# Optimization experiments

Measured on AMD Instinct MI355X. Metric: run time of the kernel, lower is better.

## Reference

```python
import jax, jax.numpy as jnp
import numpy as np

LOG_2PI = float(np.log(2.0 * np.pi))


def setup_inputs() -> dict:
    key = jax.random.key(0)
    k1, k2, k3 = jax.random.split(key, 3)
    N, M, D = 8192, 4096, 784
    samples = jax.random.normal(k1, (N, D), dtype=jnp.float32)
    x = jax.random.normal(k2, (M, D), dtype=jnp.float32)
    # per-feature std, kept away from zero for numerical sanity
    std = jax.random.uniform(k3, (D,), dtype=jnp.float32, minval=0.5, maxval=1.5)
    return {"samples": samples, "x": x, "std": std}


def reference(samples, x, std):
    # Diagonal-Gaussian mixture log-prob:
    #   logp[n, m] = sum_d [ -0.5*((s_nd - x_md)/std_d)^2 - 0.5*log(2*pi) - log(std_d) ]
    # computed via the ||u||^2 + ||v||^2 - 2 u.v identity on std-scaled vectors
    # (mathematically identical to the torch broadcast, without the (N,M,D) tensor).
    N, D = samples.shape
    M = x.shape[0]
    u = samples / std  # (N, D)
    v = x / std        # (M, D)
    sq_dist = (
        jnp.sum(u * u, axis=1)[:, None]
        + jnp.sum(v * v, axis=1)[None, :]
        - 2.0 * jnp.einsum("nd,md->nm", u, v)
    )  # (N, M)
    log_const = -0.5 * D * LOG_2PI - jnp.sum(jnp.log(std))
    log_prob = -0.5 * sq_dist + log_const  # (N, M)
    # logsumexp over mixture components, minus log(M)
    return jax.nn.logsumexp(log_prob, axis=1) - jnp.log(jnp.asarray(M, dtype=samples.dtype))
```

## Files before the change

kernel.cpp:

```cpp
#include <hip/hip_runtime.h>
#include <cstdint>
#include <cstddef>


#define N_ROWS 8192
#define M_ROWS 4096
#define D_DIM  784
#define KPB    896
#define LOG2PI 1.8378770664093453f
#define LOGM   8.317766166719343f

typedef unsigned char u8;
typedef __attribute__((ext_vector_type(8))) int   i32x8;
typedef __attribute__((ext_vector_type(4))) float f32x4;

__device__ __forceinline__ void gld16(const u8* g, u8* l) {
    __builtin_amdgcn_global_load_lds(
        (__attribute__((address_space(1))) void*)(void*)g,
        (__attribute__((address_space(3))) void*)l, 16, 0, 0);
}

__global__ __launch_bounds__(256) void k_prep(const float* __restrict__ samples,
                                              const float* __restrict__ x,
                                              const float* __restrict__ stdv,
                                              u8* __restrict__ dst,
                                              float* __restrict__ norm) {
    const int wid = threadIdx.x >> 6, lane = threadIdx.x & 63;
    const int row0 = blockIdx.x * 8 + wid * 2;

    float4 rstd[4];
#pragma unroll
    for (int i = 0; i < 4; ++i) {
        int c = lane + 64 * i;
        rstd[i] = make_float4(1.f, 1.f, 1.f, 1.f);
        if (c < 196) {
            float4 d = ((const float4*)stdv)[c];
            rstd[i] = make_float4(1.f / d.x, 1.f / d.y, 1.f / d.z, 1.f / d.w);
        }
    }

#pragma unroll
    for (int rr = 0; rr < 2; ++rr) {
        const int row = row0 + rr;
        const float* src = (row < N_ROWS) ? samples + (size_t)row * D_DIM
                                          : x + (size_t)(row - N_ROWS) * D_DIM;
        unsigned* drow = (unsigned*)(dst + (size_t)row * KPB);
        float sq = 0.f;
#pragma unroll
        for (int i = 0; i < 4; ++i) {
            const int c = lane + 64 * i;
            if (c < 224) {
                unsigned p = 0;
                if (c < 196) {
                    float4 s = ((const float4*)src)[c];
                    float ux = s.x * rstd[i].x, uy = s.y * rstd[i].y;
                    float uz = s.z * rstd[i].z, uw = s.w * rstd[i].w;
                    p = __builtin_amdgcn_cvt_pk_fp8_f32(ux, uy, 0, false);
                    p = __builtin_amdgcn_cvt_pk_fp8_f32(uz, uw, p, true);
                    float r0 = __builtin_amdgcn_cvt_f32_fp8(p, 0);
                    float r1 = __builtin_amdgcn_cvt_f32_fp8(p, 1);
                    float r2 = __builtin_amdgcn_cvt_f32_fp8(p, 2);
                    float r3 = __builtin_amdgcn_cvt_f32_fp8(p, 3);
                    sq += r0 * r0 + r1 * r1 + r2 * r2 + r3 * r3;
                }
                drow[c] = p;
            }
        }
        for (int m = 32; m; m >>= 1) sq += __shfl_xor(sq, m);
        if (lane == 0) norm[row] = sq;
    }
}

__global__ __launch_bounds__(256) void k_gemm(const u8* __restrict__ U,
                                              const u8* __restrict__ V,
                                              const float* __restrict__ vnorm,
                                              float* __restrict__ pmax,
                                              float* __restrict__ psum) {
    __shared__ __align__(16) char smem[65536];
    float2* part = (float2*)smem;

    const int tid = threadIdx.x;
    const int lane = tid & 63;
    const int wid = tid >> 6;
    const int waveRow = wid >> 1;
    const int waveCol = wid & 1;
    const int bCol = blockIdx.x;
    const int bRow = blockIdx.y;
    const int g = lane >> 4, rl = lane & 15;

    const int r16 = lane >> 2, sl = lane & 3;
    const int gc16 = sl ^ ((r16 >> 1) & 3);
    const u8* ga[4]; const u8* gb[4]; int loff[4];
#pragma unroll
    for (int t = 0; t < 4; ++t) {
        const int lin = wid * 4 + t, h = lin & 1, rg = lin >> 1;
        ga[t] = U + (size_t)(bRow * 128 + rg * 16 + r16) * KPB + h * 64 + gc16 * 16;
        gb[t] = V + (size_t)(bCol * 128 + rg * 16 + r16) * KPB + h * 64 + gc16 * 16;
        loff[t] = h * 8192 + rg * 1024;
    }

    const int key = (rl >> 1) & 3;
    const int hA = (g >> 1) * 8192;
    const int slotLo = (2 * (g & 1)) ^ key;
    const int aoff = hA + (waveRow * 64 + rl) * 64 + slotLo * 16;
    const int boff = 16384 + hA + (waveCol * 64 + rl) * 64 + slotLo * 16;

    f32x4 acc[4][4];
#pragma unroll
    for (int i = 0; i < 4; ++i)
#pragma unroll
        for (int j = 0; j < 4; ++j) acc[i][j] = (f32x4){0.f, 0.f, 0.f, 0.f};

#pragma unroll
    for (int t = 0; t < 4; ++t) gld16(ga[t], (u8*)(smem + loff[t]));
#pragma unroll
    for (int t = 0; t < 4; ++t) gld16(gb[t], (u8*)(smem + 16384 + loff[t]));

#pragma unroll
    for (int kt = 0; kt < 7; ++kt) {
        if (kt < 6) {
            char* nb = smem + ((kt + 1) & 1) * 32768;
            const int k1 = (kt + 1) * 128;
#pragma unroll
            for (int t = 0; t < 4; ++t) gld16(ga[t] + k1, (u8*)(nb + loff[t]));
#pragma unroll
            for (int t = 0; t < 4; ++t) gld16(gb[t] + k1, (u8*)(nb + 16384 + loff[t]));
            __builtin_amdgcn_s_waitcnt(0x0F78);
        } else {
            __builtin_amdgcn_s_waitcnt(0x0F70);
        }
        __builtin_amdgcn_s_barrier();

        const char* base = smem + (kt & 1) * 32768;
        i32x8 a[4], b[4];
#pragma unroll
        for (int i = 0; i < 4; ++i) {
            int4 L = *(const int4*)(base + (aoff + i * 1024));
            int4 H = *(const int4*)(base + ((aoff + i * 1024) ^ 16));
            a[i] = (i32x8){L.x, L.y, L.z, L.w, H.x, H.y, H.z, H.w};
        }
#pragma unroll
        for (int j = 0; j < 4; ++j) {
            int4 L = *(const int4*)(base + (boff + j * 1024));
            int4 H = *(const int4*)(base + ((boff + j * 1024) ^ 16));
            b[j] = (i32x8){L.x, L.y, L.z, L.w, H.x, H.y, H.z, H.w};
        }
#pragma unroll
        for (int i = 0; i < 4; ++i)
#pragma unroll
            for (int j = 0; j < 4; ++j)
                acc[i][j] = __builtin_amdgcn_mfma_scale_f32_16x16x128_f8f6f4(
                    a[i], b[j], acc[i][j], 0 , 0 ,
                    0, 127 , 0, 127 );

        __builtin_amdgcn_s_barrier();
    }
    __syncthreads();

    float vn[4];
#pragma unroll
    for (int j = 0; j < 4; ++j) vn[j] = vnorm[bCol * 128 + waveCol * 64 + j * 16 + rl];

    const int prow0 = waveRow * 64 + g * 4;
    const int pcol = waveCol * 16 + rl;
#pragma unroll
    for (int i = 0; i < 4; ++i) {
#pragma unroll
        for (int rg = 0; rg < 4; ++rg) {
            float w0 = acc[i][0][rg] - 0.5f * vn[0];
            float w1 = acc[i][1][rg] - 0.5f * vn[1];
            float w2 = acc[i][2][rg] - 0.5f * vn[2];
            float w3 = acc[i][3][rg] - 0.5f * vn[3];
            float m = fmaxf(fmaxf(w0, w1), fmaxf(w2, w3));
            float s = __expf(w0 - m) + __expf(w1 - m) + __expf(w2 - m) + __expf(w3 - m);
            part[(prow0 + i * 16 + rg) * 33 + pcol] = make_float2(m, s);
        }
    }
    __syncthreads();
    if (tid < 128) {
        const float2* p = part + tid * 33;
        float m = p[0].x;
#pragma unroll
        for (int c = 1; c < 32; ++c) m = fmaxf(m, p[c].x);
        float s = 0.f;
#pragma unroll
        for (int c = 0; c < 32; ++c) { float2 q = p[c]; s += q.y * __expf(q.x - m); }
        size_t grow = (size_t)(bRow * 128 + tid);
        pmax[grow * 32 + bCol] = m;
        psum[grow * 32 + bCol] = s;
    }
}

__global__ __launch_bounds__(256) void k_final(const float* __restrict__ pmax,
                                               const float* __restrict__ psum,
                                               const float* __restrict__ norm,
                                               const float* __restrict__ stdv,
                                               float* __restrict__ out) {
    __shared__ float wsum[4];
    const int t = threadIdx.x;
    float ls = 0.f;
    for (int d = t; d < D_DIM; d += 256) ls += logf(stdv[d]);
    for (int m = 32; m; m >>= 1) ls += __shfl_xor(ls, m);
    if ((t & 63) == 0) wsum[t >> 6] = ls;
    __syncthreads();
    const float logc = -0.5f * (float)D_DIM * LOG2PI - (wsum[0] + wsum[1] + wsum[2] + wsum[3]);

    const int n = blockIdx.x * 256 + t;
    const float* pm = pmax + (size_t)n * 32;
    const float* ps = psum + (size_t)n * 32;
    float gm = pm[0];
#pragma unroll
    for (int c = 1; c < 32; ++c) gm = fmaxf(gm, pm[c]);
    float S = 0.f;
#pragma unroll
    for (int c = 0; c < 32; ++c) S += ps[c] * __expf(pm[c] - gm);
    out[n] = gm + logf(S) - 0.5f * norm[n] + logc - LOGM;
}

extern "C" void kernel_launch(void* const* d_in, const int* in_sizes, int n_in,
                              void* d_out, int out_size, void* d_ws, size_t ws_size,
                              hipStream_t stream) {
    const float* samples = (const float*)d_in[0];
    const float* x       = (const float*)d_in[1];
    const float* stdv    = (const float*)d_in[2];
    float* out = (float*)d_out;

    char* ws = (char*)d_ws;
    u8*    U    = (u8*)ws;
    u8*    V    = (u8*)(ws + 7340032);
    float* norm = (float*)(ws + 11010048);
    float* pmax = (float*)(ws + 11059200);
    float* psum = (float*)(ws + 12107776);

    k_prep<<<(N_ROWS + M_ROWS) / 8, 256, 0, stream>>>(samples, x, stdv, U, norm);
    k_gemm<<<dim3(M_ROWS / 128, N_ROWS / 128), 256, 0, stream>>>(U, V, norm + N_ROWS, pmax, psum);
    k_final<<<N_ROWS / 256, 256, 0, stream>>>(pmax, psum, norm, stdv, out);
}
```

Before: 124.3 us.

## Enlarge GEMM tile to 256x256 with single-buffered LDS and shuffle-based epilogue

The fused FP8 GEMM+logsumexp kernel moves from 128x128 to 256x256 block tiles, with each wave computing a 128x128 sub-tile (8x8 MFMA accumulators). This raises arithmetic intensity and data reuse. LDS double buffering is replaced by a single buffer: fragments are loaded into registers, then the next K-slice is prefetched while the MFMAs run. The epilogue now reduces max and sum with cross-lane shuffles and writes per-wave partials directly instead of staging them in LDS. The grid becomes 16x32 = 512 blocks, at most one per CU under the launch bounds, and each thread holds 256 accumulator floats, so register spilling and low occupancy are real risks.

```diff
diff --git a/kernel.cpp b/kernel.cpp
--- a/kernel.cpp
+++ b/kernel.cpp
@@ -71,123 +71,110 @@
     }
 }
 
-__global__ __launch_bounds__(256) void k_gemm(const u8* __restrict__ U,
-                                              const u8* __restrict__ V,
-                                              const float* __restrict__ vnorm,
-                                              float* __restrict__ pmax,
-                                              float* __restrict__ psum) {
+__global__ __launch_bounds__(256, 1) void k_gemm(const u8* __restrict__ U,
+                                                 const u8* __restrict__ V,
+                                                 const float* __restrict__ vnorm,
+                                                 float* __restrict__ pmax,
+                                                 float* __restrict__ psum) {
     __shared__ __align__(16) char smem[65536];
-    float2* part = (float2*)smem;
 
     const int tid = threadIdx.x;
     const int lane = tid & 63;
     const int wid = tid >> 6;
-    const int waveRow = wid >> 1;
-    const int waveCol = wid & 1;
+    const int wRow = wid >> 1;
+    const int wCol = wid & 1;
     const int bCol = blockIdx.x;
     const int bRow = blockIdx.y;
     const int g = lane >> 4, rl = lane & 15;
 
-    const int r16 = lane >> 2, sl = lane & 3;
-    const int gc16 = sl ^ ((r16 >> 1) & 3);
-    const u8* ga[4]; const u8* gb[4]; int loff[4];
-#pragma unroll
-    for (int t = 0; t < 4; ++t) {
-        const int lin = wid * 4 + t, h = lin & 1, rg = lin >> 1;
-        ga[t] = U + (size_t)(bRow * 128 + rg * 16 + r16) * KPB + h * 64 + gc16 * 16;
-        gb[t] = V + (size_t)(bCol * 128 + rg * 16 + r16) * KPB + h * 64 + gc16 * 16;
-        loff[t] = h * 8192 + rg * 1024;
-    }
-
-    const int key = (rl >> 1) & 3;
-    const int hA = (g >> 1) * 8192;
-    const int slotLo = (2 * (g & 1)) ^ key;
-    const int aoff = hA + (waveRow * 64 + rl) * 64 + slotLo * 16;
-    const int boff = 16384 + hA + (waveCol * 64 + rl) * 64 + slotLo * 16;
-
-    f32x4 acc[4][4];
-#pragma unroll
-    for (int i = 0; i < 4; ++i)
-#pragma unroll
-        for (int j = 0; j < 4; ++j) acc[i][j] = (f32x4){0.f, 0.f, 0.f, 0.f};
-
-#pragma unroll
-    for (int t = 0; t < 4; ++t) gld16(ga[t], (u8*)(smem + loff[t]));
-#pragma unroll
-    for (int t = 0; t < 4; ++t) gld16(gb[t], (u8*)(smem + 16384 + loff[t]));
+    const int sr = lane >> 3;
+    const int gc16 = (lane & 7) ^ (2 * (sr & 3));
+    const u8* gaB = U + (size_t)(bRow * 256 + wid * 64 + sr) * KPB + gc16 * 16;
+    const u8* gbB = V + (size_t)(bCol * 256 + wid * 64 + sr) * KPB + gc16 * 16;
+    u8* laB = (u8*)(smem + wid * 8192);
+    u8* lbB = (u8*)(smem + 32768 + wid * 8192);
+
+    const int q = g ^ (rl & 3);
+    const int aoff = rl * 128 + q * 32;
+    const char* aB = smem + wRow * 16384;
+    const char* bB = smem + 32768 + wCol * 16384;
+
+    f32x4 acc[8][8];
+#pragma unroll
+    for (int i = 0; i < 8; ++i)
+#pragma unroll
+        for (int j = 0; j < 8; ++j) acc[i][j] = (f32x4){0.f, 0.f, 0.f, 0.f};
+
+#pragma unroll
+    for (int t = 0; t < 8; ++t) gld16(gaB + (size_t)t * 8 * KPB, laB + t * 1024);
+#pragma unroll
+    for (int t = 0; t < 8; ++t) gld16(gbB + (size_t)t * 8 * KPB, lbB + t * 1024);
 
 #pragma unroll
     for (int kt = 0; kt < 7; ++kt) {
+        __builtin_amdgcn_s_waitcnt(0x0F70);
+        __builtin_amdgcn_s_barrier();
+
+        i32x8 a[8], b[8];
+#pragma unroll
+        for (int i = 0; i < 8; ++i) {
+            int4 L = *(const int4*)(aB + aoff + i * 2048);
+            int4 H = *(const int4*)(aB + aoff + i * 2048 + 16);
+            a[i] = (i32x8){L.x, L.y, L.z, L.w, H.x, H.y, H.z, H.w};
+        }
+#pragma unroll
+        for (int j = 0; j < 8; ++j) {
+            int4 L = *(const int4*)(bB + aoff + j * 2048);
+            int4 H = *(const int4*)(bB + aoff + j * 2048 + 16);
+            b[j] = (i32x8){L.x, L.y, L.z, L.w, H.x, H.y, H.z, H.w};
+        }
+        __builtin_amdgcn_s_waitcnt(0xC07F);
+        __builtin_amdgcn_s_barrier();
+
         if (kt < 6) {
-            char* nb = smem + ((kt + 1) & 1) * 32768;
             const int k1 = (kt + 1) * 128;
 #pragma unroll
-            for (int t = 0; t < 4; ++t) gld16(ga[t] + k1, (u8*)(nb + loff[t]));
-#pragma unroll
-            for (int t = 0; t < 4; ++t) gld16(gb[t] + k1, (u8*)(nb + 16384 + loff[t]));
-            __builtin_amdgcn_s_waitcnt(0x0F78);
-        } else {
-            __builtin_amdgcn_s_waitcnt(0x0F70);
-        }
-        __builtin_amdgcn_s_barrier();
-
-        const char* base = smem + (kt & 1) * 32768;
-        i32x8 a[4], b[4];
-#pragma unroll
-        for (int i = 0; i < 4; ++i) {
-            int4 L = *(const int4*)(base + (aoff + i * 1024));
-            int4 H = *(const int4*)(base + ((aoff + i * 1024) ^ 16));
-            a[i] = (i32x8){L.x, L.y, L.z, L.w, H.x, H.y, H.z, H.w};
-        }
-#pragma unroll
-        for (int j = 0; j < 4; ++j) {
-            int4 L = *(const int4*)(base + (boff + j * 1024));
-            int4 H = *(const int4*)(base + ((boff + j * 1024) ^ 16));
-            b[j] = (i32x8){L.x, L.y, L.z, L.w, H.x, H.y, H.z, H.w};
-        }
-#pragma unroll
-        for (int i = 0; i < 4; ++i)
-#pragma unroll
-            for (int j = 0; j < 4; ++j)
+            for (int t = 0; t < 8; ++t) gld16(gaB + (size_t)t * 8 * KPB + k1, laB + t * 1024);
+#pragma unroll
+            for (int t = 0; t < 8; ++t) gld16(gbB + (size_t)t * 8 * KPB + k1, lbB + t * 1024);
+        }
+
+#pragma unroll
+        for (int i = 0; i < 8; ++i)
+#pragma unroll
+            for (int j = 0; j < 8; ++j)
                 acc[i][j] = __builtin_amdgcn_mfma_scale_f32_16x16x128_f8f6f4(
                     a[i], b[j], acc[i][j], 0 , 0 ,
                     0, 127 , 0, 127 );
-
-        __builtin_amdgcn_s_barrier();
-    }
-    __syncthreads();
-
-    float vn[4];
-#pragma unroll
-    for (int j = 0; j < 4; ++j) vn[j] = vnorm[bCol * 128 + waveCol * 64 + j * 16 + rl];
-
-    const int prow0 = waveRow * 64 + g * 4;
-    const int pcol = waveCol * 16 + rl;
-#pragma unroll
-    for (int i = 0; i < 4; ++i) {
-#pragma unroll
-        for (int rg = 0; rg < 4; ++rg) {
-            float w0 = acc[i][0][rg] - 0.5f * vn[0];
-            float w1 = acc[i][1][rg] - 0.5f * vn[1];
-            float w2 = acc[i][2][rg] - 0.5f * vn[2];
-            float w3 = acc[i][3][rg] - 0.5f * vn[3];
-            float m = fmaxf(fmaxf(w0, w1), fmaxf(w2, w3));
-            float s = __expf(w0 - m) + __expf(w1 - m) + __expf(w2 - m) + __expf(w3 - m);
-            part[(prow0 + i * 16 + rg) * 33 + pcol] = make_float2(m, s);
-        }
-    }
-    __syncthreads();
-    if (tid < 128) {
-        const float2* p = part + tid * 33;
-        float m = p[0].x;
-#pragma unroll
-        for (int c = 1; c < 32; ++c) m = fmaxf(m, p[c].x);
-        float s = 0.f;
-#pragma unroll
-        for (int c = 0; c < 32; ++c) { float2 q = p[c]; s += q.y * __expf(q.x - m); }
-        size_t grow = (size_t)(bRow * 128 + tid);
-        pmax[grow * 32 + bCol] = m;
-        psum[grow * 32 + bCol] = s;
+    }
+
+    float vn[8];
+#pragma unroll
+    for (int j = 0; j < 8; ++j) vn[j] = vnorm[bCol * 256 + wCol * 128 + j * 16 + rl];
+
+#pragma unroll
+    for (int i = 0; i < 8; ++i) {
+#pragma unroll
+        for (int r = 0; r < 4; ++r) {
+            float w[8];
+#pragma unroll
+            for (int j = 0; j < 8; ++j) w[j] = acc[i][j][r] - 0.5f * vn[j];
+            float m = w[0];
+#pragma unroll
+            for (int j = 1; j < 8; ++j) m = fmaxf(m, w[j]);
+#pragma unroll
+            for (int msk = 1; msk < 16; msk <<= 1) m = fmaxf(m, __shfl_xor(m, msk));
+            float s = 0.f;
+#pragma unroll
+            for (int j = 0; j < 8; ++j) s += __expf(w[j] - m);
+#pragma unroll
+            for (int msk = 1; msk < 16; msk <<= 1) s += __shfl_xor(s, msk);
+            if (rl == 0) {
+                size_t grow = (size_t)(bRow * 256 + wRow * 128 + i * 16 + g * 4 + r);
+                pmax[grow * 32 + bCol * 2 + wCol] = m;
+                psum[grow * 32 + bCol * 2 + wCol] = s;
+            }
+        }
     }
 }
 
@@ -233,6 +220,6 @@
     float* psum = (float*)(ws + 12107776);
 
     k_prep<<<(N_ROWS + M_ROWS) / 8, 256, 0, stream>>>(samples, x, stdv, U, norm);
-    k_gemm<<<dim3(M_ROWS / 128, N_ROWS / 128), 256, 0, stream>>>(U, V, norm + N_ROWS, pmax, psum);
+    k_gemm<<<dim3(M_ROWS / 256, N_ROWS / 256), 256, 0, stream>>>(U, V, norm + N_ROWS, pmax, psum);
     k_final<<<N_ROWS / 256, 256, 0, stream>>>(pmax, psum, norm, stdv, out);
 }
```

Result: slower. 273.5 us (+120.0%).

## Load A operand directly into registers, stage only B through LDS

Applied to the files above, without the earlier changes.

The GEMM kernel no longer stages the U (A) tile through shared memory. Each wave loads its A fragments straight from global memory into double-buffered registers, while only the V (B) tile goes through LDS. This halves LDS use, which could raise occupancy, and drops the A-side LDS reads, at the cost of uncoalesced 16-byte global loads and more registers. The prep kernel also changes to one row per wave, dividing by std directly instead of precomputing reciprocals, and launches twice as many blocks.

```diff
diff --git a/kernel.cpp b/kernel.cpp
--- a/kernel.cpp
+++ b/kernel.cpp
@@ -26,49 +26,34 @@
                                               u8* __restrict__ dst,
                                               float* __restrict__ norm) {
     const int wid = threadIdx.x >> 6, lane = threadIdx.x & 63;
-    const int row0 = blockIdx.x * 8 + wid * 2;
-
-    float4 rstd[4];
+    const int row = blockIdx.x * 4 + wid;
+    const float* src = (row < N_ROWS) ? samples + (size_t)row * D_DIM
+                                      : x + (size_t)(row - N_ROWS) * D_DIM;
+    unsigned* drow = (unsigned*)(dst + (size_t)row * KPB);
+    float sq = 0.f;
 #pragma unroll
     for (int i = 0; i < 4; ++i) {
-        int c = lane + 64 * i;
-        rstd[i] = make_float4(1.f, 1.f, 1.f, 1.f);
-        if (c < 196) {
-            float4 d = ((const float4*)stdv)[c];
-            rstd[i] = make_float4(1.f / d.x, 1.f / d.y, 1.f / d.z, 1.f / d.w);
-        }
-    }
-
-#pragma unroll
-    for (int rr = 0; rr < 2; ++rr) {
-        const int row = row0 + rr;
-        const float* src = (row < N_ROWS) ? samples + (size_t)row * D_DIM
-                                          : x + (size_t)(row - N_ROWS) * D_DIM;
-        unsigned* drow = (unsigned*)(dst + (size_t)row * KPB);
-        float sq = 0.f;
-#pragma unroll
-        for (int i = 0; i < 4; ++i) {
-            const int c = lane + 64 * i;
-            if (c < 224) {
-                unsigned p = 0;
-                if (c < 196) {
-                    float4 s = ((const float4*)src)[c];
-                    float ux = s.x * rstd[i].x, uy = s.y * rstd[i].y;
-                    float uz = s.z * rstd[i].z, uw = s.w * rstd[i].w;
-                    p = __builtin_amdgcn_cvt_pk_fp8_f32(ux, uy, 0, false);
-                    p = __builtin_amdgcn_cvt_pk_fp8_f32(uz, uw, p, true);
-                    float r0 = __builtin_amdgcn_cvt_f32_fp8(p, 0);
-                    float r1 = __builtin_amdgcn_cvt_f32_fp8(p, 1);
-                    float r2 = __builtin_amdgcn_cvt_f32_fp8(p, 2);
-                    float r3 = __builtin_amdgcn_cvt_f32_fp8(p, 3);
-                    sq += r0 * r0 + r1 * r1 + r2 * r2 + r3 * r3;
-                }
-                drow[c] = p;
+        const int c = lane + 64 * i;
+        if (c < 224) {
+            unsigned p = 0;
+            if (c < 196) {
+                float4 s = ((const float4*)src)[c];
+                float4 d = ((const float4*)stdv)[c];
+                float ux = s.x / d.x, uy = s.y / d.y;
+                float uz = s.z / d.z, uw = s.w / d.w;
+                p = __builtin_amdgcn_cvt_pk_fp8_f32(ux, uy, 0, false);
+                p = __builtin_amdgcn_cvt_pk_fp8_f32(uz, uw, p, true);
+                float r0 = __builtin_amdgcn_cvt_f32_fp8(p, 0);
+                float r1 = __builtin_amdgcn_cvt_f32_fp8(p, 1);
+                float r2 = __builtin_amdgcn_cvt_f32_fp8(p, 2);
+                float r3 = __builtin_amdgcn_cvt_f32_fp8(p, 3);
+                sq += r0 * r0 + r1 * r1 + r2 * r2 + r3 * r3;
             }
-        }
-        for (int m = 32; m; m >>= 1) sq += __shfl_xor(sq, m);
-        if (lane == 0) norm[row] = sq;
-    }
+            drow[c] = p;
+        }
+    }
+    for (int m = 32; m; m >>= 1) sq += __shfl_xor(sq, m);
+    if (lane == 0) norm[row] = sq;
 }
 
 __global__ __launch_bounds__(256) void k_gemm(const u8* __restrict__ U,
@@ -76,7 +61,7 @@
                                               const float* __restrict__ vnorm,
                                               float* __restrict__ pmax,
                                               float* __restrict__ psum) {
-    __shared__ __align__(16) char smem[65536];
+    __shared__ __align__(16) char smem[33792];
     float2* part = (float2*)smem;
 
     const int tid = threadIdx.x;
@@ -90,20 +75,20 @@
 
     const int r16 = lane >> 2, sl = lane & 3;
     const int gc16 = sl ^ ((r16 >> 1) & 3);
-    const u8* ga[4]; const u8* gb[4]; int loff[4];
+    const u8* gb[4]; int loffB[4];
 #pragma unroll
     for (int t = 0; t < 4; ++t) {
         const int lin = wid * 4 + t, h = lin & 1, rg = lin >> 1;
-        ga[t] = U + (size_t)(bRow * 128 + rg * 16 + r16) * KPB + h * 64 + gc16 * 16;
         gb[t] = V + (size_t)(bCol * 128 + rg * 16 + r16) * KPB + h * 64 + gc16 * 16;
-        loff[t] = h * 8192 + rg * 1024;
+        loffB[t] = h * 8192 + rg * 1024;
     }
 
     const int key = (rl >> 1) & 3;
-    const int hA = (g >> 1) * 8192;
+    const int hB = (g >> 1) * 8192;
     const int slotLo = (2 * (g & 1)) ^ key;
-    const int aoff = hA + (waveRow * 64 + rl) * 64 + slotLo * 16;
-    const int boff = 16384 + hA + (waveCol * 64 + rl) * 64 + slotLo * 16;
+    const int boff = hB + (waveCol * 64 + rl) * 64 + slotLo * 16;
+
+    const u8* gA = U + (size_t)(bRow * 128 + waveRow * 64 + rl) * KPB + g * 32;
 
     f32x4 acc[4][4];
 #pragma unroll
@@ -111,34 +96,34 @@
 #pragma unroll
         for (int j = 0; j < 4; ++j) acc[i][j] = (f32x4){0.f, 0.f, 0.f, 0.f};
 
-#pragma unroll
-    for (int t = 0; t < 4; ++t) gld16(ga[t], (u8*)(smem + loff[t]));
-#pragma unroll
-    for (int t = 0; t < 4; ++t) gld16(gb[t], (u8*)(smem + 16384 + loff[t]));
+    int4 aL[2][4], aH[2][4];
+
+#pragma unroll
+    for (int t = 0; t < 4; ++t) gld16(gb[t], (u8*)(smem + loffB[t]));
+#pragma unroll
+    for (int i = 0; i < 4; ++i) {
+        aL[0][i] = *(const int4*)(gA + (size_t)i * 16 * KPB);
+        aH[0][i] = *(const int4*)(gA + (size_t)i * 16 * KPB + 16);
+    }
 
 #pragma unroll
     for (int kt = 0; kt < 7; ++kt) {
+        const int cur = kt & 1, nxt = cur ^ 1;
+        __syncthreads();
         if (kt < 6) {
-            char* nb = smem + ((kt + 1) & 1) * 32768;
             const int k1 = (kt + 1) * 128;
 #pragma unroll
-            for (int t = 0; t < 4; ++t) gld16(ga[t] + k1, (u8*)(nb + loff[t]));
-#pragma unroll
-            for (int t = 0; t < 4; ++t) gld16(gb[t] + k1, (u8*)(nb + 16384 + loff[t]));
-            __builtin_amdgcn_s_waitcnt(0x0F78);
-        } else {
-            __builtin_amdgcn_s_waitcnt(0x0F70);
-        }
-        __builtin_amdgcn_s_barrier();
-
-        const char* base = smem + (kt & 1) * 32768;
-        i32x8 a[4], b[4];
-#pragma unroll
-        for (int i = 0; i < 4; ++i) {
-            int4 L = *(const int4*)(base + (aoff + i * 1024));
-            int4 H = *(const int4*)(base + ((aoff + i * 1024) ^ 16));
-            a[i] = (i32x8){L.x, L.y, L.z, L.w, H.x, H.y, H.z, H.w};
-        }
+            for (int t = 0; t < 4; ++t)
+                gld16(gb[t] + k1, (u8*)(smem + nxt * 16384 + loffB[t]));
+#pragma unroll
+            for (int i = 0; i < 4; ++i) {
+                aL[nxt][i] = *(const int4*)(gA + (size_t)i * 16 * KPB + k1);
+                aH[nxt][i] = *(const int4*)(gA + (size_t)i * 16 * KPB + k1 + 16);
+            }
+        }
+
+        const char* base = smem + cur * 16384;
+        i32x8 b[4];
 #pragma unroll
         for (int j = 0; j < 4; ++j) {
             int4 L = *(const int4*)(base + (boff + j * 1024));
@@ -146,14 +131,15 @@
             b[j] = (i32x8){L.x, L.y, L.z, L.w, H.x, H.y, H.z, H.w};
         }
 #pragma unroll
-        for (int i = 0; i < 4; ++i)
+        for (int i = 0; i < 4; ++i) {
+            i32x8 a = (i32x8){aL[cur][i].x, aL[cur][i].y, aL[cur][i].z, aL[cur][i].w,
+                              aH[cur][i].x, aH[cur][i].y, aH[cur][i].z, aH[cur][i].w};
 #pragma unroll
             for (int j = 0; j < 4; ++j)
                 acc[i][j] = __builtin_amdgcn_mfma_scale_f32_16x16x128_f8f6f4(
-                    a[i], b[j], acc[i][j], 0 , 0 ,
+                    a, b[j], acc[i][j], 0 , 0 ,
                     0, 127 , 0, 127 );
-
-        __builtin_amdgcn_s_barrier();
+        }
     }
     __syncthreads();
 
@@ -232,7 +218,7 @@
     float* pmax = (float*)(ws + 11059200);
     float* psum = (float*)(ws + 12107776);
 
-    k_prep<<<(N_ROWS + M_ROWS) / 8, 256, 0, stream>>>(samples, x, stdv, U, norm);
+    k_prep<<<(N_ROWS + M_ROWS) / 4, 256, 0, stream>>>(samples, x, stdv, U, norm);
     k_gemm<<<dim3(M_ROWS / 128, N_ROWS / 128), 256, 0, stream>>>(U, V, norm + N_ROWS, pmax, psum);
     k_final<<<N_ROWS / 256, 256, 0, stream>>>(pmax, psum, norm, stdv, out);
 }
```

Measured after the change: 153.7 us. 1.24x slower.

## Replace XOR-swizzled LDS tile layout with linear row-major subtiles; simplify prep

Applied to the files above, without the earlier changes.

In the GEMM kernel, the XOR-swizzled LDS layout for the fp8 A and B tiles is replaced by a linear layout. Each global_load_lds instruction now fills a contiguous 1 KB block of 16 rows by 64 bytes. Fragment reads become fixed offsets (+256 for the high half, 2048 between row groups) instead of XOR addressing, which simplifies index arithmetic but may change LDS bank-conflict behaviour and global coalescing. The prep kernel now handles one row per wave instead of two, divides by std directly instead of using precomputed reciprocals, and launches twice as many blocks.

```diff
diff --git a/kernel.cpp b/kernel.cpp
--- a/kernel.cpp
+++ b/kernel.cpp
@@ -26,49 +26,34 @@
                                               u8* __restrict__ dst,
                                               float* __restrict__ norm) {
     const int wid = threadIdx.x >> 6, lane = threadIdx.x & 63;
-    const int row0 = blockIdx.x * 8 + wid * 2;
-
-    float4 rstd[4];
+    const int row = blockIdx.x * 4 + wid;
+    const float* src = (row < N_ROWS) ? samples + (size_t)row * D_DIM
+                                      : x + (size_t)(row - N_ROWS) * D_DIM;
+    unsigned* drow = (unsigned*)(dst + (size_t)row * KPB);
+    float sq = 0.f;
 #pragma unroll
     for (int i = 0; i < 4; ++i) {
-        int c = lane + 64 * i;
-        rstd[i] = make_float4(1.f, 1.f, 1.f, 1.f);
-        if (c < 196) {
-            float4 d = ((const float4*)stdv)[c];
-            rstd[i] = make_float4(1.f / d.x, 1.f / d.y, 1.f / d.z, 1.f / d.w);
-        }
-    }
-
-#pragma unroll
-    for (int rr = 0; rr < 2; ++rr) {
-        const int row = row0 + rr;
-        const float* src = (row < N_ROWS) ? samples + (size_t)row * D_DIM
-                                          : x + (size_t)(row - N_ROWS) * D_DIM;
-        unsigned* drow = (unsigned*)(dst + (size_t)row * KPB);
-        float sq = 0.f;
-#pragma unroll
-        for (int i = 0; i < 4; ++i) {
-            const int c = lane + 64 * i;
-            if (c < 224) {
-                unsigned p = 0;
-                if (c < 196) {
-                    float4 s = ((const float4*)src)[c];
-                    float ux = s.x * rstd[i].x, uy = s.y * rstd[i].y;
-                    float uz = s.z * rstd[i].z, uw = s.w * rstd[i].w;
-                    p = __builtin_amdgcn_cvt_pk_fp8_f32(ux, uy, 0, false);
-                    p = __builtin_amdgcn_cvt_pk_fp8_f32(uz, uw, p, true);
-                    float r0 = __builtin_amdgcn_cvt_f32_fp8(p, 0);
-                    float r1 = __builtin_amdgcn_cvt_f32_fp8(p, 1);
-                    float r2 = __builtin_amdgcn_cvt_f32_fp8(p, 2);
-                    float r3 = __builtin_amdgcn_cvt_f32_fp8(p, 3);
-                    sq += r0 * r0 + r1 * r1 + r2 * r2 + r3 * r3;
-                }
-                drow[c] = p;
+        const int c = lane + 64 * i;
+        if (c < 224) {
+            unsigned p = 0;
+            if (c < 196) {
+                float4 s = ((const float4*)src)[c];
+                float4 d = ((const float4*)stdv)[c];
+                float ux = s.x / d.x, uy = s.y / d.y;
+                float uz = s.z / d.z, uw = s.w / d.w;
+                p = __builtin_amdgcn_cvt_pk_fp8_f32(ux, uy, 0, false);
+                p = __builtin_amdgcn_cvt_pk_fp8_f32(uz, uw, p, true);
+                float r0 = __builtin_amdgcn_cvt_f32_fp8(p, 0);
+                float r1 = __builtin_amdgcn_cvt_f32_fp8(p, 1);
+                float r2 = __builtin_amdgcn_cvt_f32_fp8(p, 2);
+                float r3 = __builtin_amdgcn_cvt_f32_fp8(p, 3);
+                sq += r0 * r0 + r1 * r1 + r2 * r2 + r3 * r3;
             }
-        }
-        for (int m = 32; m; m >>= 1) sq += __shfl_xor(sq, m);
-        if (lane == 0) norm[row] = sq;
-    }
+            drow[c] = p;
+        }
+    }
+    for (int m = 32; m; m >>= 1) sq += __shfl_xor(sq, m);
+    if (lane == 0) norm[row] = sq;
 }
 
 __global__ __launch_bounds__(256) void k_gemm(const u8* __restrict__ U,
@@ -88,22 +73,20 @@
     const int bRow = blockIdx.y;
     const int g = lane >> 4, rl = lane & 15;
 
-    const int r16 = lane >> 2, sl = lane & 3;
-    const int gc16 = sl ^ ((r16 >> 1) & 3);
+    const int srow = lane & 15;
+    const int sc16 = lane >> 4;
     const u8* ga[4]; const u8* gb[4]; int loff[4];
 #pragma unroll
     for (int t = 0; t < 4; ++t) {
-        const int lin = wid * 4 + t, h = lin & 1, rg = lin >> 1;
-        ga[t] = U + (size_t)(bRow * 128 + rg * 16 + r16) * KPB + h * 64 + gc16 * 16;
-        gb[t] = V + (size_t)(bCol * 128 + rg * 16 + r16) * KPB + h * 64 + gc16 * 16;
-        loff[t] = h * 8192 + rg * 1024;
-    }
-
-    const int key = (rl >> 1) & 3;
-    const int hA = (g >> 1) * 8192;
-    const int slotLo = (2 * (g & 1)) ^ key;
-    const int aoff = hA + (waveRow * 64 + rl) * 64 + slotLo * 16;
-    const int boff = 16384 + hA + (waveCol * 64 + rl) * 64 + slotLo * 16;
+        const int lin = wid * 4 + t, h = lin & 1, R = lin >> 1;
+        ga[t] = U + (size_t)(bRow * 128 + R * 16 + srow) * KPB + h * 64 + sc16 * 16;
+        gb[t] = V + (size_t)(bCol * 128 + R * 16 + srow) * KPB + h * 64 + sc16 * 16;
+        loff[t] = lin * 1024;
+    }
+
+    const int fo = (g >> 1) * 1024 + (g & 1) * 512 + rl * 16;
+    const int aoff = waveRow * 8192 + fo;
+    const int boff = 16384 + waveCol * 8192 + fo;
 
     f32x4 acc[4][4];
 #pragma unroll
@@ -135,14 +118,14 @@
         i32x8 a[4], b[4];
 #pragma unroll
         for (int i = 0; i < 4; ++i) {
-            int4 L = *(const int4*)(base + (aoff + i * 1024));
-            int4 H = *(const int4*)(base + ((aoff + i * 1024) ^ 16));
+            int4 L = *(const int4*)(base + (aoff + i * 2048));
+            int4 H = *(const int4*)(base + (aoff + i * 2048 + 256));
             a[i] = (i32x8){L.x, L.y, L.z, L.w, H.x, H.y, H.z, H.w};
         }
 #pragma unroll
         for (int j = 0; j < 4; ++j) {
-            int4 L = *(const int4*)(base + (boff + j * 1024));
-            int4 H = *(const int4*)(base + ((boff + j * 1024) ^ 16));
+            int4 L = *(const int4*)(base + (boff + j * 2048));
+            int4 H = *(const int4*)(base + (boff + j * 2048 + 256));
             b[j] = (i32x8){L.x, L.y, L.z, L.w, H.x, H.y, H.z, H.w};
         }
 #pragma unroll
@@ -232,7 +215,7 @@
     float* pmax = (float*)(ws + 11059200);
     float* psum = (float*)(ws + 12107776);
 
-    k_prep<<<(N_ROWS + M_ROWS) / 8, 256, 0, stream>>>(samples, x, stdv, U, norm);
+    k_prep<<<(N_ROWS + M_ROWS) / 4, 256, 0, stream>>>(samples, x, stdv, U, norm);
     k_gemm<<<dim3(M_ROWS / 128, N_ROWS / 128), 256, 0, stream>>>(U, V, norm + N_ROWS, pmax, psum);
     k_final<<<N_ROWS / 256, 256, 0, stream>>>(pmax, psum, norm, stdv, out);
 }
```

Result: slower. 149.7 us (+20.4%).
